# Kernel tuning notes

Hardware: AMD Instinct MI355X
Metric: run time of the kernel (lower is better)

Reference implementation:

```python
import jax, jax.numpy as jnp
import numpy as np

B = 16384  # batch
D = 64     # input_size (number of causal nodes)
H = 64     # hidden_size of each per-node MLP


def setup_inputs() -> dict:
    key = jax.random.key(0)
    k1, k2, k3 = jax.random.split(key, 3)
    inputs = jax.random.normal(k1, (B, D), dtype=jnp.float32)
    adjacency = jnp.ones((D, D), dtype=jnp.float32)  # buffer initialized to ones
    # stacked per-node weights: net_i = Linear(D->H, no bias) -> ReLU -> Linear(H->1, no bias)
    W1 = jax.random.normal(k2, (D, H, D), dtype=jnp.float32) * (1.0 / np.sqrt(D))
    W2 = jax.random.normal(k3, (D, H), dtype=jnp.float32) * (1.0 / np.sqrt(H))
    return {"inputs": inputs, "adjacency": adjacency, "W1": W1, "W2": W2}


def reference(inputs, adjacency, W1, W2):
    # inputs: [B, D]; adjacency: [D, D]; W1: [D, H, D]; W2: [D, H]
    # Original: repeat inputs to [B, D, D], mask rows by adjacency, then for each
    # node i apply its tiny MLP to row i and concat the scalar outputs -> [B, D].
    masked = inputs[:, None, :] * adjacency[None, :, :]          # [B, D, D]
    h = jax.nn.relu(jnp.einsum('bid,ihd->bih', masked, W1))      # [B, D, H]
    out = jnp.einsum('bih,ih->bi', h, W2)                        # [B, D]
    return out
```

## Files before the change

kernel.cpp:

```cpp
#include <hip/hip_runtime.h>
#include <hip/hip_bf16.h>

constexpr int BN = 16384;
constexpr int DN = 64;
constexpr int HN = 64;

typedef __attribute__((ext_vector_type(8))) short short8;
typedef __attribute__((ext_vector_type(4))) float f32x4;
typedef __attribute__((ext_vector_type(2))) float f32x2;

__device__ __forceinline__ unsigned short f2bf(float f) {
    __hip_bfloat16 h = __float2bfloat16(f);
    return *reinterpret_cast<unsigned short*>(&h);
}

__device__ __forceinline__ short8 cvt8(float4 a, float4 b) {
    short8 r;
    r[0] = (short)f2bf(a.x); r[1] = (short)f2bf(a.y);
    r[2] = (short)f2bf(a.z); r[3] = (short)f2bf(a.w);
    r[4] = (short)f2bf(b.x); r[5] = (short)f2bf(b.y);
    r[6] = (short)f2bf(b.z); r[7] = (short)f2bf(b.w);
    return r;
}

__global__ __launch_bounds__(256, 2) void mlp_fused_kernel(
    const float* __restrict__ X,
    const float* __restrict__ adj,
    const float* __restrict__ W1,
    const float* __restrict__ W2,
    float* __restrict__ out)
{
    const int btile = blockIdx.x & 63;
    const int ng    = blockIdx.x >> 6;
    const int tid   = threadIdx.x;
    const int wave  = tid >> 6;
    const int lane  = tid & 63;
    const int row16 = lane & 15;
    const int quad  = lane >> 4;

    __shared__ unsigned short ldsW1[4 * HN * DN];
    __shared__ unsigned short ldsX[256 * DN];
    __shared__ float ldsW2[4 * HN];

    const int b0 = btile * 256;

    {
        const float4* x4 = reinterpret_cast<const float4*>(X + (size_t)b0 * DN);
#pragma unroll
        for (int it = 0; it < 8; ++it) {
            int chunk = it * 256 + tid;
            int row = chunk >> 3;
            int c   = chunk & 7;
            float4 v0 = x4[chunk * 2];
            float4 v1 = x4[chunk * 2 + 1];
            int elem = row * 64 + ((c ^ (row & 7)) << 3);
            *reinterpret_cast<short8*>(&ldsX[elem]) = cvt8(v0, v1);
        }
    }

    {
        const float4* w4 = reinterpret_cast<const float4*>(W1 + (size_t)ng * 4 * HN * DN);
        const float4* a4 = reinterpret_cast<const float4*>(adj + (size_t)ng * 4 * DN);
#pragma unroll
        for (int it = 0; it < 8; ++it) {
            int chunk = it * 256 + tid;
            int nl = chunk >> 9;
            int h  = (chunk >> 3) & 63;
            int c  = chunk & 7;
            float4 w0 = w4[chunk * 2];
            float4 w1v = w4[chunk * 2 + 1];
            float4 a0 = a4[nl * 16 + c * 2];
            float4 a1 = a4[nl * 16 + c * 2 + 1];
            float4 m0 = {w0.x * a0.x, w0.y * a0.y, w0.z * a0.z, w0.w * a0.w};
            float4 m1 = {w1v.x * a1.x, w1v.y * a1.y, w1v.z * a1.z, w1v.w * a1.w};
            int elem = nl * 4096 + h * 64 + ((c ^ (h & 7)) << 3);
            *reinterpret_cast<short8*>(&ldsW1[elem]) = cvt8(m0, m1);
        }
        ldsW2[tid] = W2[ng * 256 + tid];
    }
    __syncthreads();

    short8 xfrag[2][4];
#pragma unroll
    for (int kk = 0; kk < 2; ++kk)
#pragma unroll
        for (int nt = 0; nt < 4; ++nt) {
            int row_l = wave * 64 + nt * 16 + row16;
            int elem = row_l * 64 + (((kk * 4 + quad) ^ (row16 & 7)) << 3);
            xfrag[kk][nt] = *reinterpret_cast<const short8*>(&ldsX[elem]);
        }

    float res[4][4];

#pragma unroll
    for (int j = 0; j < 4; ++j) {
        short8 wfrag[2][4];
#pragma unroll
        for (int kk = 0; kk < 2; ++kk)
#pragma unroll
            for (int mt = 0; mt < 4; ++mt) {
                int h = mt * 16 + row16;
                int elem = j * 4096 + h * 64 + (((kk * 4 + quad) ^ (row16 & 7)) << 3);
                wfrag[kk][mt] = *reinterpret_cast<const short8*>(&ldsW1[elem]);
            }

        float4 w2v[4];
#pragma unroll
        for (int mt = 0; mt < 4; ++mt)
            w2v[mt] = *reinterpret_cast<const float4*>(&ldsW2[j * 64 + mt * 16 + quad * 4]);

        f32x4 acc[4][4];
#pragma unroll
        for (int mt = 0; mt < 4; ++mt)
#pragma unroll
            for (int nt = 0; nt < 4; ++nt)
                acc[mt][nt] = (f32x4){0.f, 0.f, 0.f, 0.f};

#pragma unroll
        for (int kk = 0; kk < 2; ++kk)
#pragma unroll
            for (int mt = 0; mt < 4; ++mt)
#pragma unroll
                for (int nt = 0; nt < 4; ++nt)
                    acc[mt][nt] = __builtin_amdgcn_mfma_f32_16x16x32_bf16(
                        wfrag[kk][mt], xfrag[kk][nt], acc[mt][nt], 0, 0, 0);

#pragma unroll
        for (int nt = 0; nt < 4; ++nt) {
            f32x2 s = (f32x2){0.f, 0.f};
#pragma unroll
            for (int mt = 0; mt < 4; ++mt) {
                f32x2 m01 = (f32x2){fmaxf(acc[mt][nt][0], 0.f), fmaxf(acc[mt][nt][1], 0.f)};
                f32x2 m23 = (f32x2){fmaxf(acc[mt][nt][2], 0.f), fmaxf(acc[mt][nt][3], 0.f)};
                s += m01 * (f32x2){w2v[mt].x, w2v[mt].y};
                s += m23 * (f32x2){w2v[mt].z, w2v[mt].w};
            }
            float r = s[0] + s[1];
            r += __shfl_xor(r, 16);
            r += __shfl_xor(r, 32);
            res[nt][j] = r;
        }
    }

    float4 v = make_float4(0.f, 0.f, 0.f, 0.f);
#pragma unroll
    for (int nt = 0; nt < 4; ++nt)
        if (quad == nt)
            v = make_float4(res[nt][0], res[nt][1], res[nt][2], res[nt][3]);
    int row = b0 + wave * 64 + quad * 16 + row16;
    *reinterpret_cast<float4*>(out + (size_t)row * DN + ng * 4) = v;
}

extern "C" void kernel_launch(void* const* d_in, const int* in_sizes, int n_in,
                              void* d_out, int out_size, void* d_ws, size_t ws_size,
                              hipStream_t stream) {
    const float* X   = (const float*)d_in[0];
    const float* adj = (const float*)d_in[1];
    const float* W1  = (const float*)d_in[2];
    const float* W2  = (const float*)d_in[3];
    float* out = (float*)d_out;

    (void)d_ws; (void)ws_size;

    mlp_fused_kernel<<<64 * 16, 256, 0, stream>>>(X, adj, W1, W2, out);
}
```

Measured before the change: 75.88 us.

## Pre-convert inputs to swizzled bf16 in a prep kernel and load via global_load_lds

Adds a prep kernel that converts X and adjacency-masked W1 to bf16 once, already in the XOR-swizzled LDS layout, and writes them to workspace. The main kernel then fills LDS with direct global-to-LDS 16-byte loads and no longer repeats the fp32 loads and conversions in every block (each X tile was converted 16 times, each W1 group 64 times). The cost is an extra kernel launch plus a round trip through global memory for the bf16 copies.

```diff
diff --git a/kernel.cpp b/kernel.cpp
--- a/kernel.cpp
+++ b/kernel.cpp
@@ -4,6 +4,11 @@
 constexpr int BN = 16384;
 constexpr int DN = 64;
 constexpr int HN = 64;
+
+constexpr int XCHUNKS  = (BN * DN) / 8;
+constexpr int W1CHUNKS = (DN * HN * DN) / 8;
+constexpr int TOTCHUNKS = XCHUNKS + W1CHUNKS;
+constexpr int PREP_BLOCKS = TOTCHUNKS / 256;
 
 typedef __attribute__((ext_vector_type(8))) short short8;
 typedef __attribute__((ext_vector_type(4))) float f32x4;
@@ -23,10 +28,52 @@
     return r;
 }
 
+__device__ __forceinline__ void load_lds16(const unsigned short* g, unsigned short* l) {
+    __builtin_amdgcn_global_load_lds(
+        (const __attribute__((address_space(1))) unsigned int*)(const void*)g,
+        (__attribute__((address_space(3))) unsigned int*)(void*)l, 16, 0, 0);
+}
+
+__global__ __launch_bounds__(256) void prep_kernel(
+    const float* __restrict__ X, const float* __restrict__ adj,
+    const float* __restrict__ W1,
+    unsigned short* __restrict__ Xbf, unsigned short* __restrict__ W1bf)
+{
+    int c = blockIdx.x * 256 + threadIdx.x;
+    if (c < XCHUNKS) {
+        int tile = c >> 11;
+        int pos  = c & 2047;
+        int row  = pos >> 3;
+        int s    = pos & 7;
+        int col8 = s ^ (row & 7);
+        const float* p = X + ((size_t)tile * 256 + row) * DN + col8 * 8;
+        float4 v0 = *reinterpret_cast<const float4*>(p);
+        float4 v1 = *reinterpret_cast<const float4*>(p + 4);
+        reinterpret_cast<short8*>(Xbf)[c] = cvt8(v0, v1);
+    } else {
+        int c2  = c - XCHUNKS;
+        int ng  = c2 >> 11;
+        int pos = c2 & 2047;
+        int nl  = pos >> 9;
+        int h   = (pos >> 3) & 63;
+        int s   = pos & 7;
+        int col8 = s ^ (h & 7);
+        int node = ng * 4 + nl;
+        const float* wp = W1 + ((size_t)node) * HN * DN + h * DN + col8 * 8;
+        const float* ap = adj + node * DN + col8 * 8;
+        float4 w0 = *reinterpret_cast<const float4*>(wp);
+        float4 w1v = *reinterpret_cast<const float4*>(wp + 4);
+        float4 a0 = *reinterpret_cast<const float4*>(ap);
+        float4 a1 = *reinterpret_cast<const float4*>(ap + 4);
+        float4 m0 = {w0.x * a0.x, w0.y * a0.y, w0.z * a0.z, w0.w * a0.w};
+        float4 m1 = {w1v.x * a1.x, w1v.y * a1.y, w1v.z * a1.z, w1v.w * a1.w};
+        reinterpret_cast<short8*>(W1bf)[c2] = cvt8(m0, m1);
+    }
+}
+
 __global__ __launch_bounds__(256, 2) void mlp_fused_kernel(
-    const float* __restrict__ X,
-    const float* __restrict__ adj,
-    const float* __restrict__ W1,
+    const unsigned short* __restrict__ Xbf,
+    const unsigned short* __restrict__ W1bf,
     const float* __restrict__ W2,
     float* __restrict__ out)
 {
@@ -45,36 +92,13 @@
     const int b0 = btile * 256;
 
     {
-        const float4* x4 = reinterpret_cast<const float4*>(X + (size_t)b0 * DN);
+        const unsigned short* xsrc = Xbf + (size_t)btile * (256 * DN);
+        const unsigned short* wsrc = W1bf + (size_t)ng * (4 * HN * DN);
 #pragma unroll
         for (int it = 0; it < 8; ++it) {
-            int chunk = it * 256 + tid;
-            int row = chunk >> 3;
-            int c   = chunk & 7;
-            float4 v0 = x4[chunk * 2];
-            float4 v1 = x4[chunk * 2 + 1];
-            int elem = row * 64 + ((c ^ (row & 7)) << 3);
-            *reinterpret_cast<short8*>(&ldsX[elem]) = cvt8(v0, v1);
-        }
-    }
-
-    {
-        const float4* w4 = reinterpret_cast<const float4*>(W1 + (size_t)ng * 4 * HN * DN);
-        const float4* a4 = reinterpret_cast<const float4*>(adj + (size_t)ng * 4 * DN);
-#pragma unroll
-        for (int it = 0; it < 8; ++it) {
-            int chunk = it * 256 + tid;
-            int nl = chunk >> 9;
-            int h  = (chunk >> 3) & 63;
-            int c  = chunk & 7;
-            float4 w0 = w4[chunk * 2];
-            float4 w1v = w4[chunk * 2 + 1];
-            float4 a0 = a4[nl * 16 + c * 2];
-            float4 a1 = a4[nl * 16 + c * 2 + 1];
-            float4 m0 = {w0.x * a0.x, w0.y * a0.y, w0.z * a0.z, w0.w * a0.w};
-            float4 m1 = {w1v.x * a1.x, w1v.y * a1.y, w1v.z * a1.z, w1v.w * a1.w};
-            int elem = nl * 4096 + h * 64 + ((c ^ (h & 7)) << 3);
-            *reinterpret_cast<short8*>(&ldsW1[elem]) = cvt8(m0, m1);
+            int chunk = it * 256 + wave * 64;
+            load_lds16(xsrc + (size_t)(chunk + lane) * 8, &ldsX[chunk * 8]);
+            load_lds16(wsrc + (size_t)(chunk + lane) * 8, &ldsW1[chunk * 8]);
         }
         ldsW2[tid] = W2[ng * 256 + tid];
     }
@@ -160,7 +184,9 @@
     const float* W2  = (const float*)d_in[3];
     float* out = (float*)d_out;
 
-    (void)d_ws; (void)ws_size;
+    unsigned short* Xbf  = (unsigned short*)d_ws;
+    unsigned short* W1bf = (unsigned short*)d_ws + BN * DN;
 
-    mlp_fused_kernel<<<64 * 16, 256, 0, stream>>>(X, adj, W1, W2, out);
+    prep_kernel<<<PREP_BLOCKS, 256, 0, stream>>>(X, adj, W1, Xbf, W1bf);
+    mlp_fused_kernel<<<64 * 16, 256, 0, stream>>>(Xbf, W1bf, W2, out);
 }
```

Result: no change. 75.41 us (-0.6%).
